# Kernel tuning notes

Measured on AMD Instinct MI355X. Metric: run time of the kernel, lower is better.

Reference implementation:

```python
import math
import jax, jax.numpy as jnp
import numpy as np

B, C_IN, H, W = 32, 96, 64, 64
OUT = 128
EXC = int(OUT * 0.8)   # 102 excitatory channels
INH = OUT - EXC        # 26 inhibitory channels
K = 5
PAD = 2                # kernel//2 so all stages keep spatial size


def _sm_kernel(kernel_size=5, sigma_e=1.2, sigma_i=1.4):
    c = kernel_size // 2
    xx, yy = np.meshgrid(np.arange(kernel_size), np.arange(kernel_size), indexing='ij')
    xx = xx.astype(np.float32) - c
    yy = yy.astype(np.float32) - c
    ge = np.exp(-(xx ** 2 + yy ** 2) / (2 * sigma_e ** 2))
    gi = np.exp(-(xx ** 2 + yy ** 2) / (2 * sigma_i ** 2))
    dog = ge / (2 * math.pi * sigma_e ** 2) - gi / (2 * math.pi * sigma_i ** 2)
    dog = dog / dog[c, c]
    return jnp.asarray(dog[None, None], dtype=jnp.float32)  # [1,1,K,K]


def setup_inputs() -> dict:
    key = jax.random.key(0)
    k1, k2, k3, k4 = jax.random.split(key, 4)
    wr = 25.0 / math.sqrt(C_IN * K * K)
    x = jax.random.normal(k1, (B, C_IN, H, W), jnp.float32)
    w_ee = wr * jnp.abs(jax.random.normal(k2, (EXC, C_IN, K, K), jnp.float32))
    w_ei = wr * jnp.abs(jax.random.normal(k3, (INH, EXC, K, K), jnp.float32))
    w_ie = -wr * jnp.abs(jax.random.normal(k4, (EXC, INH, K, K), jnp.float32))
    return {"x": x, "w_ee": w_ee, "w_ei": w_ei, "w_ie": w_ie, "sm_kernel": _sm_kernel()}


def _reflect_pad(x, p):
    if p == 0:
        return x
    return jnp.pad(x, ((0, 0), (0, 0), (p, p), (p, p)), mode='reflect')


def _conv(x, w, pad=0, groups=1):
    return jax.lax.conv_general_dilated(
        x, w, window_strides=(1, 1), padding=[(pad, pad), (pad, pad)],
        dimension_numbers=('NCHW', 'OIHW', 'NCHW'), feature_group_count=groups)


def _forward(x, w_ee, w_ei, w_ie, sm_kernel):
    y_e = _conv(_reflect_pad(x, PAD), w_ee)                 # [B,EXC,H,W], act=Identity
    y_i = jax.nn.relu(_conv(_reflect_pad(y_e, PAD), w_ei))  # [B,INH,H,W]
    y_ie = _conv(_reflect_pad(y_i, PAD), w_ie)              # [B,EXC,H,W]
    y = y_e + y_ie
    # depthwise surround-modulation conv (zero padding, as in F.conv2d)
    w_sm = jnp.tile(sm_kernel, (EXC, 1, 1, 1))              # [EXC,1,K,K]
    y = _conv(y, w_sm, pad=K // 2, groups=EXC)
    return y, y_e, y_i


def reference(x, w_ee, w_ei, w_ie, sm_kernel):
    y, y_e, y_i = _forward(x, w_ee, w_ei, w_ie, sm_kernel)

    # --- hard WTA masks (winner channel per (b,h,w) position) ---
    win_e = jnp.argmax(y_e, axis=1)                                        # [B,H,W]
    mask_e = (jnp.arange(EXC)[None, :, None, None] == win_e[:, None]).astype(y_e.dtype)
    y_wta_e = y_e * mask_e
    win_i = jnp.argmax(jnp.abs(y_i), axis=1)
    mask_i = (jnp.arange(INH)[None, :, None, None] == win_i[:, None]).astype(y_i.dtype)
    y_wta_i = y_i * mask_i

    # --- transpose-conv outer-product trick; with same-size feature maps the
    # conv collapses to a 1x1 full correlation over (b,h,w) -> einsum ---
    yx_ee = jnp.einsum('bchw,behw->ec', x, y_wta_e)[:, :, None, None]      # [EXC,C_IN,1,1]
    yx_ei = jnp.einsum('behw,bihw->ie', y_wta_e, y_wta_i)[:, :, None, None]  # [INH,EXC,1,1]
    yx_ie = jnp.einsum('bihw,behw->ei', y_wta_i, y)[:, :, None, None]      # [EXC,INH,1,1]

    yu_e = jnp.sum(y_wta_e, axis=(0, 2, 3))[:, None, None, None]           # [EXC,1,1,1]
    yu_i = jnp.sum(jnp.abs(y_wta_i), axis=(0, 2, 3))[:, None, None, None]  # [INH,1,1,1]

    upd_ee = yx_ee - yu_e * w_ee   # broadcasts to [EXC,C_IN,K,K]
    upd_ei = yx_ei - yu_i * w_ei
    upd_ie = yx_ie - yu_e * w_ie
    upd_ee = upd_ee / (jnp.abs(upd_ee).max() + 1e-8)
    upd_ei = upd_ei / (jnp.abs(upd_ei).max() + 1e-8)
    upd_ie = upd_ie / (jnp.abs(upd_ie).max() + 1e-8)

    return (y, upd_ee, upd_ei, upd_ie)
```

## Files before the change

### kernel.cpp

```cpp
#include <hip/hip_runtime.h>

#define B_    32
#define CIN_  96
#define EXC_  102
#define INH_  26
#define HH    64
#define WW    64
#define HW_   4096
#define NPOS  (B_*HW_)
#define NPART 512
#define NEE   (EXC_*CIN_ + EXC_)
#define NIE   (EXC_*INH_)
#define N1U   (EXC_*CIN_*25)
#define N2U   (INH_*EXC_*25)
#define N3U   (EXC_*INH_*25)

typedef short bf8 __attribute__((ext_vector_type(8)));
typedef float f32x4 __attribute__((ext_vector_type(4)));

__device__ __forceinline__ int refl(int i) {
    if (i < 0) i = -i;
    if (i > 63) i = 126 - i;
    return i;
}

__device__ __forceinline__ short f2bf(float f) {
    unsigned u = __float_as_uint(f);
    return (short)((u + 0x7fffu + ((u >> 16) & 1u)) >> 16);
}

__global__ __launch_bounds__(256) void pack_all(
    const float* __restrict__ w_ee, const float* __restrict__ w_ei,
    const float* __restrict__ w_ie, const float* __restrict__ x,
    short* __restrict__ wdst, short* __restrict__ xdst,
    float* __restrict__ zreg)
{
    const int blk = blockIdx.x;
    if (blk < 1800) {
        int gi = blk*256 + threadIdx.x;
        if (gi >= 460800) return;
        const float* src; int N, C, NPAD, CPAD; int idx;
        if (gi < 268800)      { src = w_ee; N = 102; C = 96;  NPAD = 112; CPAD = 96;  idx = gi; }
        else if (gi < 371200) { src = w_ei; N = 26;  C = 102; NPAD = 32;  CPAD = 128; idx = gi - 268800; }
        else                  { src = w_ie; N = 102; C = 26;  NPAD = 112; CPAD = 32;  idx = gi - 371200; }
        int tap = idx / (NPAD*CPAD);
        int rem = idx - tap*(NPAD*CPAD);
        int n = rem / CPAD, c = rem - n*CPAD;
        float f = (n < N && c < C) ? src[((size_t)n*C + c)*25 + tap] : 0.f;
        wdst[gi] = f2bf(f);
    } else if (blk < 3848) {
        int bb = blk - 1800;
        int b = bb >> 6, bx = bb & 63;
        const int pos = bx*64 + (threadIdx.x & 63);
        const int cg0 = threadIdx.x >> 6;
        for (int cg = cg0; cg < 96/8; cg += 4) {
            bf8 v;
#pragma unroll
            for (int j = 0; j < 8; ++j)
                v[j] = f2bf(x[((size_t)b*CIN_ + cg*8 + j)*HW_ + pos]);
            *(bf8*)(&xdst[((size_t)b*HW_ + pos)*96 + cg*8]) = v;
        }
    } else {
        for (int i = threadIdx.x; i < INH_*EXC_ + INH_ + 3; i += 256) zreg[i] = 0.f;
    }
}

template<int C, int CPAD>
__global__ __launch_bounds__(256) void pack_nhwc(
    const float* __restrict__ src, short* __restrict__ dst)
{
    const int b = blockIdx.z;
    const int pos = blockIdx.x*64 + (threadIdx.x & 63);
    const int cg0 = threadIdx.x >> 6;
    for (int cg = cg0; cg < CPAD/8; cg += 4) {
        bf8 v;
#pragma unroll
        for (int j = 0; j < 8; ++j) {
            int c = cg*8 + j;
            float f = (c < C) ? src[((size_t)b*C + c)*HW_ + pos] : 0.f;
            v[j] = f2bf(f);
        }
        *(bf8*)(&dst[((size_t)b*HW_ + pos)*CPAD + cg*8]) = v;
    }
}

template<int CPAD, int NPAD, int NT, int COUT, int NCHUNK,
         bool RELU, bool ADDIN, bool WFLOAT, int OCPAD, bool WTA>
__global__ __launch_bounds__(256, 2) void conv_mfma(
    const short* __restrict__ src, const short* __restrict__ wgt,
    const float* __restrict__ addin, float* __restrict__ out,
    short* __restrict__ nhwc_out, int* __restrict__ win,
    float* __restrict__ val)
{
    __shared__ __align__(16) short sA[400*40];
    const int t  = threadIdx.x;
    const int bx = blockIdx.x;
    const int b  = blockIdx.z;
    const int h0 = (bx >> 2) * 16;
    const int w0 = (bx &  3) * 16;
    const int lane = t & 63;
    const int wv = t >> 6;
    const int nh = lane & 15;
    const int q  = lane >> 4;

    int goff[7], loff[7];
#pragma unroll
    for (int s = 0; s < 7; ++s) {
        int i = t + 256*s;
        if (i < 1600) {
            int rec = i >> 2, seg = i & 3;
            int lh = rec / 20, lw = rec - lh*20;
            int gh = refl(h0 - 2 + lh), gw = refl(w0 - 2 + lw);
            goff[s] = (b*HW_ + gh*WW + gw) * CPAD + seg*8;
            loff[s] = rec*40 + seg*8;
        } else { goff[s] = 0; loff[s] = -1; }
    }

    f32x4 acc[4][NT];
#pragma unroll
    for (int mt = 0; mt < 4; ++mt)
#pragma unroll
        for (int nt = 0; nt < NT; ++nt) {
            f32x4 z = {0.f, 0.f, 0.f, 0.f};
            acc[mt][nt] = z;
        }

    int abase[4];
#pragma unroll
    for (int mt = 0; mt < 4; ++mt)
        abase[mt] = ((wv*4 + mt)*20 + nh)*40 + q*8;

    for (int ck = 0; ck < NCHUNK; ++ck) {
        const int c0 = ck*32;
        __syncthreads();
#pragma unroll
        for (int s = 0; s < 7; ++s)
            if (loff[s] >= 0)
                *(bf8*)(&sA[loff[s]]) = *(const bf8*)(&src[goff[s] + c0]);
        __syncthreads();
        const short* wch = wgt + c0 + nh*CPAD + q*8;
        for (int dh = 0; dh < 5; ++dh) {
#pragma unroll
            for (int dw = 0; dw < 5; ++dw) {
                const int tap = dh*5 + dw;
                bf8 bfr[NT];
#pragma unroll
                for (int nt = 0; nt < NT; ++nt)
                    bfr[nt] = *(const bf8*)(&wch[(size_t)(tap*NPAD + nt*16)*CPAD]);
                bf8 afr[4];
#pragma unroll
                for (int mt = 0; mt < 4; ++mt)
                    afr[mt] = *(const bf8*)(&sA[abase[mt] + (dh*20 + dw)*40]);
#pragma unroll
                for (int mt = 0; mt < 4; ++mt)
#pragma unroll
                    for (int nt = 0; nt < NT; ++nt)
                        acc[mt][nt] = __builtin_amdgcn_mfma_f32_16x16x32_bf16(
                            afr[mt], bfr[nt], acc[mt][nt], 0, 0, 0);
            }
        }
    }

#pragma unroll
    for (int mt = 0; mt < 4; ++mt) {
        const int rowi = h0 + wv*4 + mt;
#pragma unroll
        for (int nt = 0; nt < NT; ++nt) {
            const int chn = nt*16 + nh;
            if (WFLOAT && chn < COUT) {
                size_t obase = ((size_t)(b*COUT + chn))*HW_ + rowi*WW + w0 + q*4;
#pragma unroll
                for (int r = 0; r < 4; ++r) {
                    float v = acc[mt][nt][r];
                    if (RELU) v = fmaxf(v, 0.f);
                    if (ADDIN) v += addin[obase + r];
                    out[obase + r] = v;
                }
            }
            if (OCPAD > 0) {
#pragma unroll
                for (int r = 0; r < 4; ++r) {
                    float v = acc[mt][nt][r];
                    if (RELU) v = fmaxf(v, 0.f);
                    int pos = rowi*WW + w0 + q*4 + r;
                    nhwc_out[((size_t)b*HW_ + pos)*OCPAD + chn] = f2bf(v);
                }
            }
        }
        if (OCPAD > NT*16) {
#pragma unroll
            for (int r = 0; r < 4; ++r) {
                int pos = rowi*WW + w0 + q*4 + r;
                for (int ct = NT*16 + nh; ct < OCPAD; ct += 16)
                    nhwc_out[((size_t)b*HW_ + pos)*OCPAD + ct] = 0;
            }
        }
        if (WTA) {
#pragma unroll
            for (int r = 0; r < 4; ++r) {
                float bv = -3.402823e38f; int bc = 0;
#pragma unroll
                for (int nt = 0; nt < NT; ++nt) {
                    const int chn = nt*16 + nh;
                    float v = acc[mt][nt][r];
                    if (RELU) v = fmaxf(v, 0.f);
                    if (chn < COUT && v > bv) { bv = v; bc = chn; }
                }
#pragma unroll
                for (int off = 1; off < 16; off <<= 1) {
                    float ov = __shfl_xor(bv, off);
                    int   oc = __shfl_xor(bc, off);
                    if (ov > bv || (ov == bv && oc < bc)) { bv = ov; bc = oc; }
                }
                if (nh == 0) {
                    int p = b*HW_ + rowi*WW + w0 + q*4 + r;
                    win[p] = bc; val[p] = bv;
                }
            }
        }
    }
}

__global__ __launch_bounds__(256) void smconv_v2(
    const float* __restrict__ in, const float* __restrict__ sm,
    float* __restrict__ out)
{
    __shared__ __align__(16) float sx[36*36];
    const int tid = threadIdx.x;
    const int tile = blockIdx.x;
    const int e = blockIdx.y;
    const int b = blockIdx.z;
    const int h0 = (tile >> 1) * 32, w0 = (tile & 1) * 32;
    const int r  = tid >> 3;
    const int cg = (tid & 7) * 4;
    const float* inc = in + ((size_t)(b*EXC_ + e))*HW_;
#pragma unroll
    for (int it = 0; it < 6; ++it) {
        int i = tid + it*256;
        if (i < 1296) {
            int lh = i / 36, lw = i - lh*36;
            int gh = h0 - 2 + lh, gw = w0 - 2 + lw;
            float v = 0.f;
            if (gh >= 0 && gh < HH && gw >= 0 && gw < WW) v = inc[gh*WW + gw];
            sx[i] = v;
        }
    }
    __syncthreads();
    float a0 = 0.f, a1 = 0.f, a2 = 0.f, a3 = 0.f;
#pragma unroll
    for (int kh = 0; kh < 5; ++kh) {
        const float4* rowp = (const float4*)(sx + (r + kh)*36 + cg);
        float4 v0 = rowp[0], v1 = rowp[1];
        float xv[8] = {v0.x, v0.y, v0.z, v0.w, v1.x, v1.y, v1.z, v1.w};
#pragma unroll
        for (int kw = 0; kw < 5; ++kw) {
            float wv = sm[kh*5 + kw];
            a0 = fmaf(xv[kw+0], wv, a0);
            a1 = fmaf(xv[kw+1], wv, a1);
            a2 = fmaf(xv[kw+2], wv, a2);
            a3 = fmaf(xv[kw+3], wv, a3);
        }
    }
    size_t oidx = ((size_t)(b*EXC_ + e))*HW_ + (h0 + r)*WW + w0 + cg;
    *(float4*)(out + oidx) = make_float4(a0, a1, a2, a3);
}

__global__ __launch_bounds__(256) void scatter_ee_kernel(
    const float* __restrict__ x, const int* __restrict__ win_e,
    const float* __restrict__ val_e, float* __restrict__ parts)
{
    __shared__ float s_yx[EXC_*CIN_];
    __shared__ float s_yu[EXC_];
    __shared__ float s_xs[CIN_*33];
    __shared__ float s_val[256];
    __shared__ int   s_win[256];
    const int t = threadIdx.x;
    for (int i = t; i < EXC_*CIN_; i += 256) s_yx[i] = 0.f;
    if (t < EXC_) s_yu[t] = 0.f;
    {
        int p = blockIdx.x*256 + t;
        s_win[t] = win_e[p];
        s_val[t] = val_e[p];
    }
    const int p0  = blockIdx.x * 256;
    const int b   = p0 >> 12;
    const int hw0 = p0 & 4095;
    const float* xb = x + (size_t)b*CIN_*HW_ + hw0;
    const int c = (t < 96) ? t : t - 96;
    const int h = (t < 96) ? 0 : 1;

    for (int ch = 0; ch < 8; ++ch) {
        __syncthreads();
#pragma unroll
        for (int it = 0; it < 3; ++it) {
            int idx = t + it*256;
            if (idx < 768) {
                int cr = idx >> 3, c4 = idx & 7;
                float4 v = *(const float4*)(xb + (size_t)cr*HW_ + ch*32 + c4*4);
                float* d = &s_xs[cr*33 + c4*4];
                d[0] = v.x; d[1] = v.y; d[2] = v.z; d[3] = v.w;
            }
        }
        __syncthreads();
        if (t < 192) {
#pragma unroll
            for (int k = 0; k < 16; ++k) {
                int pos = ch*32 + h*16 + k;
                float ve = s_val[pos]; int we = s_win[pos];
                atomicAdd(&s_yx[we*CIN_ + c], ve * s_xs[c*33 + h*16 + k]);
                if (c == 0) atomicAdd(&s_yu[we], ve);
            }
        }
    }
    __syncthreads();
    float* dee = parts + (size_t)blockIdx.x * NEE;
    for (int i = t; i < EXC_*CIN_; i += 256) dee[i] = s_yx[i];
    if (t < EXC_) dee[EXC_*CIN_ + t] = s_yu[t];
}

__global__ __launch_bounds__(256) void scatter_iei_kernel(
    const float* __restrict__ y, const int* __restrict__ win_e,
    const float* __restrict__ val_e, const int* __restrict__ win_i,
    const float* __restrict__ val_i, float* __restrict__ yx_ei,
    float* __restrict__ yu_i, float* __restrict__ parts)
{
    __shared__ float s_ie[EXC_*27];
    __shared__ float s_ei[INH_*EXC_ + INH_];
    __shared__ float s_ys[EXC_*33];
    __shared__ float s_val[256];
    __shared__ int   s_win[256];
    const int t = threadIdx.x;
    for (int i = t; i < EXC_*27; i += 256) s_ie[i] = 0.f;
    for (int i = t; i < INH_*EXC_ + INH_; i += 256) s_ei[i] = 0.f;
    {
        int p = blockIdx.x*256 + t;
        s_win[t] = win_i[p];
        s_val[t] = val_i[p];
    }
    __syncthreads();

    {
        int p = blockIdx.x*256 + t;
        int we = win_e[p]; float ve = val_e[p];
        int wi = s_win[t]; float vi = s_val[t];
        atomicAdd(&s_ei[wi*EXC_ + we], ve*vi);
        atomicAdd(&s_ei[INH_*EXC_ + wi], fabsf(vi));
    }

    const int p0  = blockIdx.x * 256;
    const int b   = p0 >> 12;
    const int hw0 = p0 & 4095;
    const float* yb = y + (size_t)b*EXC_*HW_ + hw0;
    const int e = (t < 102) ? t : t - 102;
    const int h = (t < 102) ? 0 : 1;

    for (int ch = 0; ch < 8; ++ch) {
        __syncthreads();
#pragma unroll
        for (int it = 0; it < 4; ++it) {
            int idx = t + it*256;
            if (idx < 816) {
                int er = idx >> 3, c4 = idx & 7;
                float4 v = *(const float4*)(yb + (size_t)er*HW_ + ch*32 + c4*4);
                float* d = &s_ys[er*33 + c4*4];
                d[0] = v.x; d[1] = v.y; d[2] = v.z; d[3] = v.w;
            }
        }
        __syncthreads();
        if (t < 204) {
#pragma unroll
            for (int k = 0; k < 16; ++k) {
                int pos = ch*32 + h*16 + k;
                float vi = s_val[pos];
                if (vi != 0.f) {
                    int wi = s_win[pos];
                    atomicAdd(&s_ie[e*27 + wi], vi * s_ys[e*33 + h*16 + k]);
                }
            }
        }
    }
    __syncthreads();

    for (int i = t; i < INH_*EXC_ + INH_; i += 256) {
        float v = s_ei[i];
        if (v != 0.f) {
            if (i < INH_*EXC_) atomicAdd(&yx_ei[i], v);
            else               atomicAdd(&yu_i[i - INH_*EXC_], v);
        }
    }
    float* die = parts + (size_t)blockIdx.x * NIE;
    for (int i = t; i < EXC_*INH_; i += 256) {
        int ee = i / INH_, ii = i - ee*INH_;
        die[i] = s_ie[ee*27 + ii];
    }
}

__global__ __launch_bounds__(256) void reduce_all_kernel(
    const float* __restrict__ parts_ee, const float* __restrict__ parts_ie,
    float* __restrict__ yx_ee, float* __restrict__ yx_ie)
{
    __shared__ float s[256];
    int col = blockIdx.x*64 + (threadIdx.x & 63);
    int g = threadIdx.x >> 6;
    const float* P; float* D; int n, i;
    if (col < NEE) { P = parts_ee; D = yx_ee; n = NEE; i = col; }
    else           { P = parts_ie; D = yx_ie; n = NIE; i = col - NEE; }
    float a = 0.f;
    if (col < NEE + NIE) {
        for (int j = g*(NPART/4); j < (g+1)*(NPART/4); ++j)
            a += P[(size_t)j*n + i];
    }
    s[threadIdx.x] = a;
    __syncthreads();
    if (threadIdx.x < 64 && col < NEE + NIE)
        D[i] = s[threadIdx.x] + s[threadIdx.x+64] + s[threadIdx.x+128] + s[threadIdx.x+192];
}

__global__ __launch_bounds__(256) void upd_absmax3(
    const float* __restrict__ yx_ee, const float* __restrict__ yu_e,
    const float* __restrict__ w_ee,
    const float* __restrict__ yx_ei, const float* __restrict__ yu_i,
    const float* __restrict__ w_ei,
    const float* __restrict__ yx_ie, const float* __restrict__ w_ie,
    unsigned int* __restrict__ amax)
{
    float m0 = 0.f, m1 = 0.f, m2 = 0.f;
    for (int idx = blockIdx.x*256 + threadIdx.x; idx < N1U + N2U + N3U;
         idx += gridDim.x*256) {
        if (idx < N1U) {
            int ec = idx / 25; int e = ec / CIN_;
            m0 = fmaxf(m0, fabsf(yx_ee[ec] - yu_e[e]*w_ee[idx]));
        } else if (idx < N1U + N2U) {
            int j = idx - N1U; int ec = j / 25; int e = ec / EXC_;
            m1 = fmaxf(m1, fabsf(yx_ei[ec] - yu_i[e]*w_ei[j]));
        } else {
            int j = idx - N1U - N2U; int ec = j / 25; int e = ec / INH_;
            m2 = fmaxf(m2, fabsf(yx_ie[ec] - yu_e[e]*w_ie[j]));
        }
    }
    __shared__ unsigned int s0, s1, s2;
    if (threadIdx.x == 0) { s0 = 0u; s1 = 0u; s2 = 0u; }
    __syncthreads();
    atomicMax(&s0, __float_as_uint(m0));
    atomicMax(&s1, __float_as_uint(m1));
    atomicMax(&s2, __float_as_uint(m2));
    __syncthreads();
    if (threadIdx.x == 0) {
        atomicMax(&amax[0], s0);
        atomicMax(&amax[1], s1);
        atomicMax(&amax[2], s2);
    }
}

__global__ __launch_bounds__(256) void upd_write3(
    const float* __restrict__ yx_ee, const float* __restrict__ yu_e,
    const float* __restrict__ w_ee,
    const float* __restrict__ yx_ei, const float* __restrict__ yu_i,
    const float* __restrict__ w_ei,
    const float* __restrict__ yx_ie, const float* __restrict__ w_ie,
    const unsigned int* __restrict__ amax,
    float* __restrict__ out_ee, float* __restrict__ out_ei,
    float* __restrict__ out_ie)
{
    int idx = blockIdx.x*256 + threadIdx.x;
    if (idx >= N1U + N2U + N3U) return;
    if (idx < N1U) {
        int ec = idx / 25; int e = ec / CIN_;
        float v = yx_ee[ec] - yu_e[e]*w_ee[idx];
        out_ee[idx] = v / (__uint_as_float(amax[0]) + 1e-8f);
    } else if (idx < N1U + N2U) {
        int j = idx - N1U; int ec = j / 25; int e = ec / EXC_;
        float v = yx_ei[ec] - yu_i[e]*w_ei[j];
        out_ei[j] = v / (__uint_as_float(amax[1]) + 1e-8f);
    } else {
        int j = idx - N1U - N2U; int ec = j / 25; int e = ec / INH_;
        float v = yx_ie[ec] - yu_e[e]*w_ie[j];
        out_ie[j] = v / (__uint_as_float(amax[2]) + 1e-8f);
    }
}

extern "C" void kernel_launch(void* const* d_in, const int* in_sizes, int n_in,
                              void* d_out, int out_size, void* d_ws, size_t ws_size,
                              hipStream_t stream)
{
    const float* x    = (const float*)d_in[0];
    const float* w_ee = (const float*)d_in[1];
    const float* w_ei = (const float*)d_in[2];
    const float* w_ie = (const float*)d_in[3];
    const float* smk  = (const float*)d_in[4];
    float* out = (float*)d_out;

    const size_t SZ_YE   = (size_t)B_*EXC_*HW_;
    const size_t SZ_YEBF = (size_t)B_*HW_*128;
    const size_t SZ_XBF  = (size_t)B_*HW_*96;
    const size_t SZ_W    = 460800;
    const size_t need_direct =
        SZ_YE*4 + SZ_YEBF*2 + SZ_XBF*2 + SZ_W*2 + (size_t)NPOS*16 + 16000*4;
    const bool direct = (ws_size >= need_direct);

    float* y_e  = (float*)d_ws;
    short* yebf; short* R;
    if (direct) {
        yebf = (short*)(y_e + SZ_YE);
        R    = yebf + SZ_YEBF;
    } else {
        yebf = nullptr;
        R    = (short*)(y_e + SZ_YE);
    }
    short* yibf = direct ? R : R;
    short* bigR = direct ? R : (R + (size_t)B_*HW_*32);
    short* wee  = direct ? (R + SZ_XBF) : (bigR + (size_t)16777216);
    short* wei  = wee + 268800;
    short* wie  = wei + 102400;
    int*   win_e = (int*)(wie + 89600);
    float* val_e = (float*)(win_e + NPOS);
    int*   win_i = (int*)(val_e + NPOS);
    float* val_i = (float*)(win_i + NPOS);
    float* yx_ee = val_i + NPOS;
    float* yu_e  = yx_ee + EXC_*CIN_;
    float* yx_ie = yu_e + EXC_;
    float* yx_ei = yx_ie + EXC_*INH_;
    float* yu_i  = yx_ei + INH_*EXC_;
    unsigned int* amax = (unsigned int*)(yu_i + INH_);
    float* parts_ee = y_e;
    float* parts_ie = parts_ee + (size_t)NPART*NEE;

    pack_all<<<3849, 256, 0, stream>>>(w_ee, w_ei, w_ie, x, wee, bigR, yx_ei);

    if (direct) {
        conv_mfma<96, 112, 7, EXC_, 3, false, false, true, 128, true>
            <<<dim3(16, 1, B_), 256, 0, stream>>>(bigR, wee, nullptr, y_e, yebf,
                                                  win_e, val_e);
        conv_mfma<128, 32, 2, INH_, 4, true, false, false, 32, true>
            <<<dim3(16, 1, B_), 256, 0, stream>>>(yebf, wei, nullptr, nullptr,
                                                  yibf, win_i, val_i);
        conv_mfma<32, 112, 7, EXC_, 1, false, true, true, 0, false>
            <<<dim3(16, 1, B_), 256, 0, stream>>>(yibf, wie, y_e, y_e, nullptr,
                                                  nullptr, nullptr);
    } else {
        conv_mfma<96, 112, 7, EXC_, 3, false, false, true, 0, true>
            <<<dim3(16, 1, B_), 256, 0, stream>>>(bigR, wee, nullptr, y_e, nullptr,
                                                  win_e, val_e);
        pack_nhwc<EXC_, 128><<<dim3(64, 1, B_), 256, 0, stream>>>(y_e, bigR);
        conv_mfma<128, 32, 2, INH_, 4, true, false, false, 32, true>
            <<<dim3(16, 1, B_), 256, 0, stream>>>(bigR, wei, nullptr, nullptr,
                                                  yibf, win_i, val_i);
        conv_mfma<32, 112, 7, EXC_, 1, false, true, true, 0, false>
            <<<dim3(16, 1, B_), 256, 0, stream>>>(yibf, wie, y_e, y_e, nullptr,
                                                  nullptr, nullptr);
    }

    smconv_v2<<<dim3(4, EXC_, B_), 256, 0, stream>>>(y_e, smk, out);

    scatter_ee_kernel<<<NPART, 256, 0, stream>>>(x, win_e, val_e, parts_ee);
    scatter_iei_kernel<<<NPART, 256, 0, stream>>>(out, win_e, val_e, win_i,
                                                  val_i, yx_ei, yu_i, parts_ie);

    reduce_all_kernel<<<(NEE + NIE + 63)/64, 256, 0, stream>>>(
        parts_ee, parts_ie, yx_ee, yx_ie);

    upd_absmax3<<<480, 256, 0, stream>>>(yx_ee, yu_e, w_ee, yx_ei, yu_i, w_ei,
                                         yx_ie, w_ie, amax);
    float* out_ee = out + (size_t)B_*EXC_*HW_;
    float* out_ei = out_ee + N1U;
    float* out_ie = out_ei + N2U;
    upd_write3<<<(N1U + N2U + N3U + 255)/256, 256, 0, stream>>>(
        yx_ee, yu_e, w_ee, yx_ei, yu_i, w_ei, yx_ie, w_ie, amax,
        out_ee, out_ei, out_ie);
}
```

Baseline: 561.0 us.

## Remap scatter kernels to per-position threads and fuse reduce with absmax

The two scatter kernels now assign one spatial position per thread, using a permuted index to spread LDS atomic conflicts, and loop over channel chunks instead of giving each thread one channel. Shared tiles are padded to reduce bank conflicts. The partial-sum reduction and the absmax pass are merged into one kernel, removing a launch and a re-read of the reduced sums. Atomic contention on s_yx now depends on how many positions pick the same winner, and yu_e is read from the partials rather than a precomputed array.

Measured after the change: 534.0 us. -4.8%, faster.

```diff
diff --git a/kernel.cpp b/kernel.cpp
--- a/kernel.cpp
+++ b/kernel.cpp
@@ -11,6 +11,7 @@
 #define NPART 512
 #define NEE   (EXC_*CIN_ + EXC_)
 #define NIE   (EXC_*INH_)
+#define NEI   (INH_*EXC_)
 #define N1U   (EXC_*CIN_*25)
 #define N2U   (INH_*EXC_*25)
 #define N3U   (EXC_*INH_*25)
@@ -269,52 +270,46 @@
     const float* __restrict__ x, const int* __restrict__ win_e,
     const float* __restrict__ val_e, float* __restrict__ parts)
 {
-    __shared__ float s_yx[EXC_*CIN_];
+    __shared__ float s_yx[EXC_*97];
     __shared__ float s_yu[EXC_];
-    __shared__ float s_xs[CIN_*33];
+    __shared__ float s_xs[16*258];
     __shared__ float s_val[256];
     __shared__ int   s_win[256];
     const int t = threadIdx.x;
-    for (int i = t; i < EXC_*CIN_; i += 256) s_yx[i] = 0.f;
+    for (int i = t; i < EXC_*97; i += 256) s_yx[i] = 0.f;
     if (t < EXC_) s_yu[t] = 0.f;
     {
         int p = blockIdx.x*256 + t;
         s_win[t] = win_e[p];
         s_val[t] = val_e[p];
     }
+    __syncthreads();
+    const int pp = (t*75) & 255;
+    const int myw = s_win[pp];
+    const float myv = s_val[pp];
+    atomicAdd(&s_yu[myw], myv);
+
     const int p0  = blockIdx.x * 256;
     const int b   = p0 >> 12;
     const int hw0 = p0 & 4095;
     const float* xb = x + (size_t)b*CIN_*HW_ + hw0;
-    const int c = (t < 96) ? t : t - 96;
-    const int h = (t < 96) ? 0 : 1;
-
-    for (int ch = 0; ch < 8; ++ch) {
+
+    for (int ch = 0; ch < 6; ++ch) {
         __syncthreads();
 #pragma unroll
-        for (int it = 0; it < 3; ++it) {
-            int idx = t + it*256;
-            if (idx < 768) {
-                int cr = idx >> 3, c4 = idx & 7;
-                float4 v = *(const float4*)(xb + (size_t)cr*HW_ + ch*32 + c4*4);
-                float* d = &s_xs[cr*33 + c4*4];
-                d[0] = v.x; d[1] = v.y; d[2] = v.z; d[3] = v.w;
-            }
-        }
+        for (int it = 0; it < 16; ++it)
+            s_xs[it*258 + t] = xb[(size_t)(ch*16 + it)*HW_ + t];
         __syncthreads();
-        if (t < 192) {
-#pragma unroll
-            for (int k = 0; k < 16; ++k) {
-                int pos = ch*32 + h*16 + k;
-                float ve = s_val[pos]; int we = s_win[pos];
-                atomicAdd(&s_yx[we*CIN_ + c], ve * s_xs[c*33 + h*16 + k]);
-                if (c == 0) atomicAdd(&s_yu[we], ve);
-            }
-        }
+#pragma unroll
+        for (int c = 0; c < 16; ++c)
+            atomicAdd(&s_yx[myw*97 + ch*16 + c], myv * s_xs[c*258 + pp]);
     }
     __syncthreads();
     float* dee = parts + (size_t)blockIdx.x * NEE;
-    for (int i = t; i < EXC_*CIN_; i += 256) dee[i] = s_yx[i];
+    for (int i = t; i < EXC_*CIN_; i += 256) {
+        int e = i / CIN_, c = i - e*CIN_;
+        dee[i] = s_yx[e*97 + c];
+    }
     if (t < EXC_) dee[EXC_*CIN_ + t] = s_yu[t];
 }
 
@@ -326,7 +321,7 @@
 {
     __shared__ float s_ie[EXC_*27];
     __shared__ float s_ei[INH_*EXC_ + INH_];
-    __shared__ float s_ys[EXC_*33];
+    __shared__ float s_ys[17*258];
     __shared__ float s_val[256];
     __shared__ int   s_win[256];
     const int t = threadIdx.x;
@@ -338,49 +333,34 @@
         s_val[t] = val_i[p];
     }
     __syncthreads();
-
+    const int pp = (t*75) & 255;
+    const int myw = s_win[pp];
+    const float myv = s_val[pp];
     {
-        int p = blockIdx.x*256 + t;
+        int p = blockIdx.x*256 + pp;
         int we = win_e[p]; float ve = val_e[p];
-        int wi = s_win[t]; float vi = s_val[t];
-        atomicAdd(&s_ei[wi*EXC_ + we], ve*vi);
-        atomicAdd(&s_ei[INH_*EXC_ + wi], fabsf(vi));
+        atomicAdd(&s_ei[myw*EXC_ + we], ve*myv);
+        atomicAdd(&s_ei[INH_*EXC_ + myw], fabsf(myv));
     }
 
     const int p0  = blockIdx.x * 256;
     const int b   = p0 >> 12;
     const int hw0 = p0 & 4095;
     const float* yb = y + (size_t)b*EXC_*HW_ + hw0;
-    const int e = (t < 102) ? t : t - 102;
-    const int h = (t < 102) ? 0 : 1;
-
-    for (int ch = 0; ch < 8; ++ch) {
+
+    for (int ch = 0; ch < 6; ++ch) {
         __syncthreads();
 #pragma unroll
-        for (int it = 0; it < 4; ++it) {
-            int idx = t + it*256;
-            if (idx < 816) {
-                int er = idx >> 3, c4 = idx & 7;
-                float4 v = *(const float4*)(yb + (size_t)er*HW_ + ch*32 + c4*4);
-                float* d = &s_ys[er*33 + c4*4];
-                d[0] = v.x; d[1] = v.y; d[2] = v.z; d[3] = v.w;
-            }
-        }
+        for (int it = 0; it < 17; ++it)
+            s_ys[it*258 + t] = yb[(size_t)(ch*17 + it)*HW_ + t];
         __syncthreads();
-        if (t < 204) {
-#pragma unroll
-            for (int k = 0; k < 16; ++k) {
-                int pos = ch*32 + h*16 + k;
-                float vi = s_val[pos];
-                if (vi != 0.f) {
-                    int wi = s_win[pos];
-                    atomicAdd(&s_ie[e*27 + wi], vi * s_ys[e*33 + h*16 + k]);
-                }
-            }
-        }
-    }
-    __syncthreads();
-
+        if (myv != 0.f) {
+#pragma unroll
+            for (int c = 0; c < 17; ++c)
+                atomicAdd(&s_ie[(ch*17 + c)*27 + myw], myv * s_ys[c*258 + pp]);
+        }
+    }
+    __syncthreads();
     for (int i = t; i < INH_*EXC_ + INH_; i += 256) {
         float v = s_ei[i];
         if (v != 0.f) {
@@ -390,65 +370,83 @@
     }
     float* die = parts + (size_t)blockIdx.x * NIE;
     for (int i = t; i < EXC_*INH_; i += 256) {
-        int ee = i / INH_, ii = i - ee*INH_;
-        die[i] = s_ie[ee*27 + ii];
-    }
-}
-
-__global__ __launch_bounds__(256) void reduce_all_kernel(
+        int e = i / INH_, ii = i - e*INH_;
+        die[i] = s_ie[e*27 + ii];
+    }
+}
+
+__global__ __launch_bounds__(256) void reduce_absmax_kernel(
     const float* __restrict__ parts_ee, const float* __restrict__ parts_ie,
-    float* __restrict__ yx_ee, float* __restrict__ yx_ie)
-{
-    __shared__ float s[256];
-    int col = blockIdx.x*64 + (threadIdx.x & 63);
-    int g = threadIdx.x >> 6;
-    const float* P; float* D; int n, i;
-    if (col < NEE) { P = parts_ee; D = yx_ee; n = NEE; i = col; }
-    else           { P = parts_ie; D = yx_ie; n = NIE; i = col - NEE; }
-    float a = 0.f;
-    if (col < NEE + NIE) {
-        for (int j = g*(NPART/4); j < (g+1)*(NPART/4); ++j)
-            a += P[(size_t)j*n + i];
-    }
-    s[threadIdx.x] = a;
-    __syncthreads();
-    if (threadIdx.x < 64 && col < NEE + NIE)
-        D[i] = s[threadIdx.x] + s[threadIdx.x+64] + s[threadIdx.x+128] + s[threadIdx.x+192];
-}
-
-__global__ __launch_bounds__(256) void upd_absmax3(
-    const float* __restrict__ yx_ee, const float* __restrict__ yu_e,
-    const float* __restrict__ w_ee,
     const float* __restrict__ yx_ei, const float* __restrict__ yu_i,
-    const float* __restrict__ w_ei,
-    const float* __restrict__ yx_ie, const float* __restrict__ w_ie,
+    const float* __restrict__ w_ee, const float* __restrict__ w_ei,
+    const float* __restrict__ w_ie,
+    float* __restrict__ yx_ee, float* __restrict__ yx_ie,
     unsigned int* __restrict__ amax)
 {
-    float m0 = 0.f, m1 = 0.f, m2 = 0.f;
-    for (int idx = blockIdx.x*256 + threadIdx.x; idx < N1U + N2U + N3U;
-         idx += gridDim.x*256) {
-        if (idx < N1U) {
-            int ec = idx / 25; int e = ec / CIN_;
-            m0 = fmaxf(m0, fabsf(yx_ee[ec] - yu_e[e]*w_ee[idx]));
-        } else if (idx < N1U + N2U) {
-            int j = idx - N1U; int ec = j / 25; int e = ec / EXC_;
-            m1 = fmaxf(m1, fabsf(yx_ei[ec] - yu_i[e]*w_ei[j]));
-        } else {
-            int j = idx - N1U - N2U; int ec = j / 25; int e = ec / INH_;
-            m2 = fmaxf(m2, fabsf(yx_ie[ec] - yu_e[e]*w_ie[j]));
-        }
-    }
-    __shared__ unsigned int s0, s1, s2;
-    if (threadIdx.x == 0) { s0 = 0u; s1 = 0u; s2 = 0u; }
-    __syncthreads();
-    atomicMax(&s0, __float_as_uint(m0));
-    atomicMax(&s1, __float_as_uint(m1));
-    atomicMax(&s2, __float_as_uint(m2));
-    __syncthreads();
-    if (threadIdx.x == 0) {
-        atomicMax(&amax[0], s0);
-        atomicMax(&amax[1], s1);
-        atomicMax(&amax[2], s2);
+    __shared__ float s[256], su[256];
+    __shared__ unsigned int sm0, sm1, sm2;
+    const int t = threadIdx.x;
+    if (t == 0) { sm0 = 0u; sm1 = 0u; sm2 = 0u; }
+    int col = blockIdx.x*64 + (t & 63);
+    int g = t >> 6;
+    float a = 0.f, ayu = 0.f;
+    if (col < NEE) {
+        int e = (col < EXC_*CIN_) ? col / CIN_ : -1;
+        for (int j = g*(NPART/4); j < (g+1)*(NPART/4); ++j) {
+            a += parts_ee[(size_t)j*NEE + col];
+            if (e >= 0) ayu += parts_ee[(size_t)j*NEE + EXC_*CIN_ + e];
+        }
+    } else if (col < NEE + NIE) {
+        int j2 = col - NEE;
+        int e = j2 / INH_;
+        for (int j = g*(NPART/4); j < (g+1)*(NPART/4); ++j) {
+            a   += parts_ie[(size_t)j*NIE + j2];
+            ayu += parts_ee[(size_t)j*NEE + EXC_*CIN_ + e];
+        }
+    }
+    s[t] = a; su[t] = ayu;
+    __syncthreads();
+    if (t < 64) {
+        float m0 = 0.f, m1 = 0.f, m2 = 0.f;
+        if (col < NEE + NIE + NEI) {
+            if (col < NEE) {
+                float yx = s[t] + s[t+64] + s[t+128] + s[t+192];
+                yx_ee[col] = yx;
+                if (col < EXC_*CIN_) {
+                    float yu = su[t] + su[t+64] + su[t+128] + su[t+192];
+                    const float* wp = w_ee + (size_t)col*25;
+#pragma unroll
+                    for (int tap = 0; tap < 25; ++tap)
+                        m0 = fmaxf(m0, fabsf(yx - yu*wp[tap]));
+                }
+            } else if (col < NEE + NIE) {
+                int j2 = col - NEE;
+                float yx = s[t] + s[t+64] + s[t+128] + s[t+192];
+                float yu = su[t] + su[t+64] + su[t+128] + su[t+192];
+                yx_ie[j2] = yx;
+                const float* wp = w_ie + (size_t)j2*25;
+#pragma unroll
+                for (int tap = 0; tap < 25; ++tap)
+                    m2 = fmaxf(m2, fabsf(yx - yu*wp[tap]));
+            } else {
+                int k = col - NEE - NIE;
+                float yx = yx_ei[k];
+                float yu = yu_i[k / EXC_];
+                const float* wp = w_ei + (size_t)k*25;
+#pragma unroll
+                for (int tap = 0; tap < 25; ++tap)
+                    m1 = fmaxf(m1, fabsf(yx - yu*wp[tap]));
+            }
+        }
+        atomicMax(&sm0, __float_as_uint(m0));
+        atomicMax(&sm1, __float_as_uint(m1));
+        atomicMax(&sm2, __float_as_uint(m2));
+    }
+    __syncthreads();
+    if (t == 0) {
+        if (sm0) atomicMax(&amax[0], sm0);
+        if (sm1) atomicMax(&amax[1], sm1);
+        if (sm2) atomicMax(&amax[2], sm2);
     }
 }
 
@@ -556,11 +554,10 @@
     scatter_iei_kernel<<<NPART, 256, 0, stream>>>(out, win_e, val_e, win_i,
                                                   val_i, yx_ei, yu_i, parts_ie);
 
-    reduce_all_kernel<<<(NEE + NIE + 63)/64, 256, 0, stream>>>(
-        parts_ee, parts_ie, yx_ee, yx_ie);
-
-    upd_absmax3<<<480, 256, 0, stream>>>(yx_ee, yu_e, w_ee, yx_ei, yu_i, w_ei,
-                                         yx_ie, w_ie, amax);
+    reduce_absmax_kernel<<<(NEE + NIE + NEI + 63)/64, 256, 0, stream>>>(
+        parts_ee, parts_ie, yx_ei, yu_i, w_ee, w_ei, w_ie,
+        yx_ee, yx_ie, amax);
+
     float* out_ee = out + (size_t)B_*EXC_*HW_;
     float* out_ei = out_ee + N1U;
     float* out_ie = out_ei + N2U;
```
